# Kernel tuning notes

Measured on AMD Instinct MI355X. Metric: run time of the kernel, lower is better.

The kernel has to match this reference:

```python
import jax, jax.numpy as jnp
import numpy as np

# Module hyperparameters (from init_kwargs)
K = 3          # kernel size
STRIDE = 1
PAD = 1
DIL = 1
DG = 1         # deformable groups
GROUPS = 1     # conv groups


def setup_inputs() -> dict:
    key = jax.random.key(0)
    k1, k2, k3, k4 = jax.random.split(key, 4)
    inputs = jax.random.normal(k1, (8, 64, 96, 96), dtype=jnp.float32)
    offset = jax.random.normal(k2, (8, DG * 2 * K * K, 96, 96), dtype=jnp.float32)
    mask = jax.random.uniform(k3, (8, DG * K * K, 96, 96), dtype=jnp.float32)
    # xavier-ish scale for the conv weight
    weight = jax.random.normal(k4, (64, 64, K, K), dtype=jnp.float32) * 0.05
    return {"inputs": inputs, "offset": offset, "mask": mask, "weight": weight}


def _bilinear_sample(xg, py, px):
    """xg: [N, dg, Cg, H, W]; py, px: [N, dg, P] fractional coords.
    Out-of-bounds samples contribute zero (DCN convention)."""
    N, dg, Cg, H, W = xg.shape
    xf = xg.reshape(N, dg, Cg, H * W)
    y0 = jnp.floor(py)
    x0 = jnp.floor(px)
    wy1 = py - y0
    wx1 = px - x0
    wy0 = 1.0 - wy1
    wx0 = 1.0 - wx1
    y0i = y0.astype(jnp.int32)
    x0i = x0.astype(jnp.int32)
    y1i = y0i + 1
    x1i = x0i + 1

    def gather(yi, xi, w):
        valid = (yi >= 0) & (yi < H) & (xi >= 0) & (xi < W)
        idx = jnp.clip(yi, 0, H - 1) * W + jnp.clip(xi, 0, W - 1)  # [N,dg,P]
        idx_b = jnp.broadcast_to(idx[:, :, None, :], (N, dg, Cg, idx.shape[-1]))
        v = jnp.take_along_axis(xf, idx_b, axis=-1)  # [N,dg,Cg,P]
        return v * (w * valid)[:, :, None, :]

    return (gather(y0i, x0i, wy0 * wx0) + gather(y0i, x1i, wy0 * wx1)
            + gather(y1i, x0i, wy1 * wx0) + gather(y1i, x1i, wy1 * wx1))


def reference(inputs, offset, mask, weight):
    N, C, H, W = inputs.shape
    Cout = weight.shape[0]
    KK = K * K
    Hout = (H + 2 * PAD - DIL * (K - 1) - 1) // STRIDE + 1
    Wout = (W + 2 * PAD - DIL * (K - 1) - 1) // STRIDE + 1

    # offset channels: per deformable group, per kernel tap, (dy, dx) interleaved
    off = offset.reshape(N, DG, KK, 2, Hout, Wout)
    m = mask.reshape(N, DG, KK, Hout, Wout)

    ky, kx = jnp.meshgrid(jnp.arange(K), jnp.arange(K), indexing="ij")
    ky = ky.reshape(KK).astype(jnp.float32)
    kx = kx.reshape(KK).astype(jnp.float32)
    gy = (jnp.arange(Hout) * STRIDE - PAD).astype(jnp.float32)
    gx = (jnp.arange(Wout) * STRIDE - PAD).astype(jnp.float32)
    base_y = ky[:, None, None] * DIL + gy[None, :, None]  # [KK,Hout,1]
    base_x = kx[:, None, None] * DIL + gx[None, None, :]  # [KK,1,Wout]

    py = off[:, :, :, 0] + base_y  # [N,DG,KK,Hout,Wout]
    px = off[:, :, :, 1] + base_x

    P = KK * Hout * Wout
    xg = inputs.reshape(N, DG, C // DG, H, W)
    sampled = _bilinear_sample(xg, py.reshape(N, DG, P), px.reshape(N, DG, P))
    sampled = sampled.reshape(N, DG, C // DG, KK, Hout, Wout) * m[:, :, None]
    cols = sampled.reshape(N, C, KK, Hout, Wout)

    # groups == 1: single GEMM over (C, KK)
    out = jnp.einsum("nckhw,ock->nohw", cols, weight.reshape(Cout, C, KK))
    return out
```

## Files before the change

### kernel.cpp

```cpp
#include <hip/hip_runtime.h>

#define HWX 9216
#define CIN 64
#define COUT 64
#define SR 14
#define SC 24
#define SLOT 144

typedef __attribute__((ext_vector_type(8))) short short8;
typedef __attribute__((ext_vector_type(8))) _Float16 half8;
typedef __attribute__((ext_vector_type(2))) _Float16 half2v;
typedef __attribute__((ext_vector_type(4))) float f32x4;
typedef __attribute__((ext_vector_type(4))) unsigned int u32x4;

__device__ inline unsigned short f2h(float f) {
    union { _Float16 h; unsigned short u; } v;
    v.h = (_Float16)f;
    return v.u;
}
__device__ inline unsigned pack2h(float lo, float hi) {
    return (unsigned)f2h(lo) | ((unsigned)f2h(hi) << 16);
}

__global__ __launch_bounds__(256) void nchw_to_nhwc_f16(const float* __restrict__ x,
                                                        unsigned* __restrict__ xt) {
    __shared__ float tile[64][65];
    int n  = blockIdx.x / 144;
    int p0 = (blockIdx.x % 144) * 64;
    const float* xp = x + (size_t)n * CIN * HWX + p0;
    #pragma unroll
    for (int it = 0; it < 16; ++it) {
        int px = threadIdx.x & 63;
        int c  = (threadIdx.x >> 6) + it * 4;
        tile[c][px] = xp[c * HWX + px];
    }
    __syncthreads();
    unsigned* xo = xt + ((size_t)n * HWX + p0) * 32;
    #pragma unroll
    for (int it = 0; it < 8; ++it) {
        int c2 = threadIdx.x & 31;
        int px = (threadIdx.x >> 5) + it * 8;
        xo[px * 32 + c2] = pack2h(tile[2 * c2][px], tile[2 * c2 + 1][px]);
    }
}

__global__ void dcn_prep_weight(const float* __restrict__ w, unsigned short* __restrict__ wA) {
    int idx = blockIdx.x * blockDim.x + threadIdx.x;
    int j    = idx & 7;
    int lane = (idx >> 3) & 63;
    int m0   = (idx >> 9) & 3;
    int step = idx >> 11;
    int co = m0 * 16 + (lane & 15);
    int kg = step * 32 + ((lane >> 4) << 3) + j;
    int kk = kg >> 6;
    int c  = kg & 63;
    wA[idx] = f2h(w[(co * 64 + c) * 9 + kk]);
}

__global__ __launch_bounds__(384, 4) void dcn_fwd(const unsigned short* __restrict__ xt,
                                                  const float* __restrict__ offset,
                                                  const float* __restrict__ mask,
                                                  const unsigned short* __restrict__ wA,
                                                  float* __restrict__ out) {
    __shared__ __align__(16) char ldsx[SR * SC * SLOT];

    int bid = blockIdx.x;
    int swz = (bid & 7) * 96 + (bid >> 3);
    int n   = swz / 96;
    int t0  = swz % 96;
    int r0  = (t0 / 6) * 6;
    int c0  = (t0 % 6) * 16;

    int sy0 = r0 - 4;
    int sx0 = c0 - 4;

    const unsigned short* xn = xt + (size_t)n * HWX * 64;

    int wave = threadIdx.x >> 6;
    int lane = threadIdx.x & 63;
    int l15  = lane & 15;
    int lg   = lane >> 4;

    int ho = r0 + wave;
    int wo = c0 + l15;

    float dyv[9], dxv[9], mv[9];
    #pragma unroll
    for (int kk = 0; kk < 9; ++kk) {
        dyv[kk] = offset[((n * 18 + 2 * kk + 0) * 96 + ho) * 96 + wo];
        dxv[kk] = offset[((n * 18 + 2 * kk + 1) * 96 + ho) * 96 + wo];
        mv[kk]  = mask[((n * 9 + kk) * 96 + ho) * 96 + wo];
    }

    #pragma unroll
    for (int it = 0; it < 7; ++it) {
        int i  = threadIdx.x + it * 384;
        int s  = i >> 3, ch = i & 7;
        int ly = s / SC, lx = s - ly * SC;
        int gy = min(max(sy0 + ly, 0), 95);
        int gx = min(max(sx0 + lx, 0), 95);
        *(u32x4*)(ldsx + s * SLOT + ch * 16) =
            *((const u32x4*)(xn + (gy * 96 + gx) * 64) + ch);
    }
    __syncthreads();

    f32x4 acc[4] = {f32x4{0,0,0,0}, f32x4{0,0,0,0}, f32x4{0,0,0,0}, f32x4{0,0,0,0}};

    #pragma unroll
    for (int kk = 0; kk < 9; ++kk) {
        int ky = kk / 3, kx = kk % 3;
        float dy = dyv[kk];
        float dx = dxv[kk];
        float m  = mv[kk];

        float py = dy + (float)(ky + ho - 1);
        float px = dx + (float)(kx + wo - 1);
        float y0f = floorf(py), x0f = floorf(px);
        float wy1 = py - y0f,  wx1 = px - x0f;
        float wy0 = 1.f - wy1, wx0 = 1.f - wx1;
        int y0 = (int)y0f, x0 = (int)x0f;
        int y1 = y0 + 1,   x1 = x0 + 1;
        bool vy0 = (y0 >= 0) && (y0 < 96);
        bool vy1 = (y1 >= 0) && (y1 < 96);
        bool vx0 = (x0 >= 0) && (x0 < 96);
        bool vx1 = (x1 >= 0) && (x1 < 96);
        int y0c = min(max(y0, 0), 95), y1c = min(max(y1, 0), 95);
        int x0c = min(max(x0, 0), 95), x1c = min(max(x1, 0), 95);
        float w00 = wy0 * wx0 * m * ((vy0 && vx0) ? 1.f : 0.f);
        float w01 = wy0 * wx1 * m * ((vy0 && vx1) ? 1.f : 0.f);
        float w10 = wy1 * wx0 * m * ((vy1 && vx0) ? 1.f : 0.f);
        float w11 = wy1 * wx1 * m * ((vy1 && vx1) ? 1.f : 0.f);

        _Float16 h00 = (_Float16)w00, h01 = (_Float16)w01;
        _Float16 h10 = (_Float16)w10, h11 = (_Float16)w11;
        half2v W00 = {h00, h00}, W01 = {h01, h01}, W10 = {h10, h10}, W11 = {h11, h11};

        bool local = (y0c >= sy0) & (y1c <= sy0 + SR - 1) &
                     (x0c >= sx0) & (x1c <= sx0 + SC - 1);
        int ly0 = min(max(y0c - sy0, 0), SR - 1);
        int ly1 = min(max(y1c - sy0, 0), SR - 1);
        int lx0 = min(max(x0c - sx0, 0), SC - 1);
        int lx1 = min(max(x1c - sx0, 0), SC - 1);
        int s00 = (ly0 * SC + lx0) * SLOT;
        int s01 = (ly0 * SC + lx1) * SLOT;
        int s10 = (ly1 * SC + lx0) * SLOT;
        int s11 = (ly1 * SC + lx1) * SLOT;

        #pragma unroll
        for (int half = 0; half < 2; ++half) {
            int step = kk * 2 + half;
            int cb   = half * 32 + lg * 8;
            int cb2  = cb * 2;

            const half8* wp = (const half8*)(wA + (step * 256 + lane) * 8);
            half8 af0 = wp[0];
            half8 af1 = wp[64];
            half8 af2 = wp[128];
            half8 af3 = wp[192];

            union { u32x4 u; half2v h[4]; } a00, a01, a10, a11, r;
            a00.u = *(const u32x4*)(ldsx + s00 + cb2);
            a01.u = *(const u32x4*)(ldsx + s01 + cb2);
            a10.u = *(const u32x4*)(ldsx + s10 + cb2);
            a11.u = *(const u32x4*)(ldsx + s11 + cb2);

            if (!local) {
                a00.u = *(const u32x4*)(xn + (y0c * 96 + x0c) * 64 + cb);
                a01.u = *(const u32x4*)(xn + (y0c * 96 + x1c) * 64 + cb);
                a10.u = *(const u32x4*)(xn + (y1c * 96 + x0c) * 64 + cb);
                a11.u = *(const u32x4*)(xn + (y1c * 96 + x1c) * 64 + cb);
            }

            #pragma unroll
            for (int p = 0; p < 4; ++p) {
                r.h[p] = a00.h[p] * W00 + a01.h[p] * W01
                       + a10.h[p] * W10 + a11.h[p] * W11;
            }
            half8 bfrag = *(half8*)&r;

            acc[0] = __builtin_amdgcn_mfma_f32_16x16x32_f16(af0, bfrag, acc[0], 0, 0, 0);
            acc[1] = __builtin_amdgcn_mfma_f32_16x16x32_f16(af1, bfrag, acc[1], 0, 0, 0);
            acc[2] = __builtin_amdgcn_mfma_f32_16x16x32_f16(af2, bfrag, acc[2], 0, 0, 0);
            acc[3] = __builtin_amdgcn_mfma_f32_16x16x32_f16(af3, bfrag, acc[3], 0, 0, 0);
        }
    }

    size_t obase = (size_t)n * COUT * HWX + (size_t)ho * 96 + wo;
    #pragma unroll
    for (int m0 = 0; m0 < 4; ++m0) {
        #pragma unroll
        for (int r = 0; r < 4; ++r) {
            int co = m0 * 16 + lg * 4 + r;
            out[obase + (size_t)co * HWX] = acc[m0][r];
        }
    }
}

extern "C" void kernel_launch(void* const* d_in, const int* in_sizes, int n_in,
                              void* d_out, int out_size, void* d_ws, size_t ws_size,
                              hipStream_t stream) {
    const float* x      = (const float*)d_in[0];
    const float* offset = (const float*)d_in[1];
    const float* mask   = (const float*)d_in[2];
    const float* w      = (const float*)d_in[3];
    float* out = (float*)d_out;
    unsigned* xt       = (unsigned*)d_ws;
    unsigned short* wA = (unsigned short*)((char*)d_ws + (size_t)8 * HWX * 64 * 2);

    hipLaunchKernelGGL(nchw_to_nhwc_f16, dim3(1152), dim3(256), 0, stream, x, xt);
    hipLaunchKernelGGL(dcn_prep_weight, dim3(144), dim3(256), 0, stream, w, wA);
    hipLaunchKernelGGL(dcn_fwd, dim3(768), dim3(384), 0, stream,
                       (const unsigned short*)xt, offset, mask, wA, out);
}
```

Baseline: 34.81 us.

## Software-pipeline bilinear gather one step ahead of MFMA accumulation

Restructures the main tap loop as a software pipeline: the LDS/global corner loads for step u are issued while step u-1's interpolation and MFMAs run, using double-buffered sample and weight registers. Offset and mask values are now loaded one tap ahead instead of all 27 up front, which lowers register pressure. The aim is to hide LDS and global load latency behind MFMA work. In exchange, the live buffers add registers and the compiler may already have scheduled the fully unrolled loop similarly.

```diff
diff --git a/kernel.cpp b/kernel.cpp
--- a/kernel.cpp
+++ b/kernel.cpp
@@ -84,14 +84,6 @@
     int ho = r0 + wave;
     int wo = c0 + l15;
 
-    float dyv[9], dxv[9], mv[9];
-    #pragma unroll
-    for (int kk = 0; kk < 9; ++kk) {
-        dyv[kk] = offset[((n * 18 + 2 * kk + 0) * 96 + ho) * 96 + wo];
-        dxv[kk] = offset[((n * 18 + 2 * kk + 1) * 96 + ho) * 96 + wo];
-        mv[kk]  = mask[((n * 9 + kk) * 96 + ho) * 96 + wo];
-    }
-
     #pragma unroll
     for (int it = 0; it < 7; ++it) {
         int i  = threadIdx.x + it * 384;
@@ -104,84 +96,101 @@
     }
     __syncthreads();
 
+    typedef union { u32x4 u; half2v h[4]; } U;
+
     f32x4 acc[4] = {f32x4{0,0,0,0}, f32x4{0,0,0,0}, f32x4{0,0,0,0}, f32x4{0,0,0,0}};
 
-    #pragma unroll
-    for (int kk = 0; kk < 9; ++kk) {
-        int ky = kk / 3, kx = kk % 3;
-        float dy = dyv[kk];
-        float dx = dxv[kk];
-        float m  = mv[kk];
-
-        float py = dy + (float)(ky + ho - 1);
-        float px = dx + (float)(kx + wo - 1);
-        float y0f = floorf(py), x0f = floorf(px);
-        float wy1 = py - y0f,  wx1 = px - x0f;
-        float wy0 = 1.f - wy1, wx0 = 1.f - wx1;
-        int y0 = (int)y0f, x0 = (int)x0f;
-        int y1 = y0 + 1,   x1 = x0 + 1;
-        bool vy0 = (y0 >= 0) && (y0 < 96);
-        bool vy1 = (y1 >= 0) && (y1 < 96);
-        bool vx0 = (x0 >= 0) && (x0 < 96);
-        bool vx1 = (x1 >= 0) && (x1 < 96);
-        int y0c = min(max(y0, 0), 95), y1c = min(max(y1, 0), 95);
-        int x0c = min(max(x0, 0), 95), x1c = min(max(x1, 0), 95);
-        float w00 = wy0 * wx0 * m * ((vy0 && vx0) ? 1.f : 0.f);
-        float w01 = wy0 * wx1 * m * ((vy0 && vx1) ? 1.f : 0.f);
-        float w10 = wy1 * wx0 * m * ((vy1 && vx0) ? 1.f : 0.f);
-        float w11 = wy1 * wx1 * m * ((vy1 && vx1) ? 1.f : 0.f);
-
-        _Float16 h00 = (_Float16)w00, h01 = (_Float16)w01;
-        _Float16 h10 = (_Float16)w10, h11 = (_Float16)w11;
-        half2v W00 = {h00, h00}, W01 = {h01, h01}, W10 = {h10, h10}, W11 = {h11, h11};
-
-        bool local = (y0c >= sy0) & (y1c <= sy0 + SR - 1) &
-                     (x0c >= sx0) & (x1c <= sx0 + SC - 1);
-        int ly0 = min(max(y0c - sy0, 0), SR - 1);
-        int ly1 = min(max(y1c - sy0, 0), SR - 1);
-        int lx0 = min(max(x0c - sx0, 0), SC - 1);
-        int lx1 = min(max(x1c - sx0, 0), SC - 1);
-        int s00 = (ly0 * SC + lx0) * SLOT;
-        int s01 = (ly0 * SC + lx1) * SLOT;
-        int s10 = (ly1 * SC + lx0) * SLOT;
-        int s11 = (ly1 * SC + lx1) * SLOT;
-
-        #pragma unroll
-        for (int half = 0; half < 2; ++half) {
-            int step = kk * 2 + half;
-            int cb   = half * 32 + lg * 8;
-            int cb2  = cb * 2;
-
-            const half8* wp = (const half8*)(wA + (step * 256 + lane) * 8);
-            half8 af0 = wp[0];
-            half8 af1 = wp[64];
-            half8 af2 = wp[128];
-            half8 af3 = wp[192];
-
-            union { u32x4 u; half2v h[4]; } a00, a01, a10, a11, r;
-            a00.u = *(const u32x4*)(ldsx + s00 + cb2);
-            a01.u = *(const u32x4*)(ldsx + s01 + cb2);
-            a10.u = *(const u32x4*)(ldsx + s10 + cb2);
-            a11.u = *(const u32x4*)(ldsx + s11 + cb2);
-
-            if (!local) {
-                a00.u = *(const u32x4*)(xn + (y0c * 96 + x0c) * 64 + cb);
-                a01.u = *(const u32x4*)(xn + (y0c * 96 + x1c) * 64 + cb);
-                a10.u = *(const u32x4*)(xn + (y1c * 96 + x0c) * 64 + cb);
-                a11.u = *(const u32x4*)(xn + (y1c * 96 + x1c) * 64 + cb);
+    U buf[2][4];
+    half2v Wt[2][4];
+    int sS0 = 0, sS1 = 0, sS2 = 0, sS3 = 0;
+    int gS0 = 0, gS1 = 0, gS2 = 0, gS3 = 0;
+    bool locS = true;
+    float dyn_, dxn_, mn_;
+
+    dyn_ = offset[((n * 18 + 0) * 96 + ho) * 96 + wo];
+    dxn_ = offset[((n * 18 + 1) * 96 + ho) * 96 + wo];
+    mn_  = mask[((n * 9 + 0) * 96 + ho) * 96 + wo];
+
+    #pragma unroll
+    for (int u = 0; u <= 18; ++u) {
+        if (u < 18) {
+            const int tp = u >> 1;
+            const int hp = u & 1;
+            if (hp == 0) {
+                float dy = dyn_, dx = dxn_, mm = mn_;
+                if (tp < 8) {
+                    dyn_ = offset[((n * 18 + 2 * (tp + 1) + 0) * 96 + ho) * 96 + wo];
+                    dxn_ = offset[((n * 18 + 2 * (tp + 1) + 1) * 96 + ho) * 96 + wo];
+                    mn_  = mask[((n * 9 + (tp + 1)) * 96 + ho) * 96 + wo];
+                }
+                float py = dy + (float)(tp / 3 + ho - 1);
+                float px = dx + (float)(tp % 3 + wo - 1);
+                float y0f = floorf(py), x0f = floorf(px);
+                float wy1 = py - y0f, wx1 = px - x0f;
+                float wy0 = 1.f - wy1, wx0 = 1.f - wx1;
+                int y0 = (int)y0f, x0 = (int)x0f;
+                int y1 = y0 + 1, x1 = x0 + 1;
+                bool vy0 = (y0 >= 0) && (y0 < 96);
+                bool vy1 = (y1 >= 0) && (y1 < 96);
+                bool vx0 = (x0 >= 0) && (x0 < 96);
+                bool vx1 = (x1 >= 0) && (x1 < 96);
+                int y0c = min(max(y0, 0), 95), y1c = min(max(y1, 0), 95);
+                int x0c = min(max(x0, 0), 95), x1c = min(max(x1, 0), 95);
+                float w00 = wy0 * wx0 * mm * ((vy0 && vx0) ? 1.f : 0.f);
+                float w01 = wy0 * wx1 * mm * ((vy0 && vx1) ? 1.f : 0.f);
+                float w10 = wy1 * wx0 * mm * ((vy1 && vx0) ? 1.f : 0.f);
+                float w11 = wy1 * wx1 * mm * ((vy1 && vx1) ? 1.f : 0.f);
+                _Float16 h00 = (_Float16)w00, h01 = (_Float16)w01;
+                _Float16 h10 = (_Float16)w10, h11 = (_Float16)w11;
+                Wt[tp & 1][0] = (half2v){h00, h00};
+                Wt[tp & 1][1] = (half2v){h01, h01};
+                Wt[tp & 1][2] = (half2v){h10, h10};
+                Wt[tp & 1][3] = (half2v){h11, h11};
+                locS = (y0c >= sy0) && (y1c <= sy0 + SR - 1) &&
+                       (x0c >= sx0) && (x1c <= sx0 + SC - 1);
+                int ly0 = min(max(y0c - sy0, 0), SR - 1);
+                int ly1 = min(max(y1c - sy0, 0), SR - 1);
+                int lx0 = min(max(x0c - sx0, 0), SC - 1);
+                int lx1 = min(max(x1c - sx0, 0), SC - 1);
+                sS0 = (ly0 * SC + lx0) * SLOT; sS1 = (ly0 * SC + lx1) * SLOT;
+                sS2 = (ly1 * SC + lx0) * SLOT; sS3 = (ly1 * SC + lx1) * SLOT;
+                gS0 = (y0c * 96 + x0c) * 64; gS1 = (y0c * 96 + x1c) * 64;
+                gS2 = (y1c * 96 + x0c) * 64; gS3 = (y1c * 96 + x1c) * 64;
             }
-
-            #pragma unroll
-            for (int p = 0; p < 4; ++p) {
-                r.h[p] = a00.h[p] * W00 + a01.h[p] * W01
-                       + a10.h[p] * W10 + a11.h[p] * W11;
+            {
+                const int oh = hp ? (64 + lg * 16) : (lg * 16);
+                buf[hp][0].u = *(const u32x4*)(ldsx + sS0 + oh);
+                buf[hp][1].u = *(const u32x4*)(ldsx + sS1 + oh);
+                buf[hp][2].u = *(const u32x4*)(ldsx + sS2 + oh);
+                buf[hp][3].u = *(const u32x4*)(ldsx + sS3 + oh);
+                if (__builtin_expect(!locS, 0)) {
+                    const int ch = hp ? (32 + lg * 8) : (lg * 8);
+                    buf[hp][0].u = *(const u32x4*)(xn + gS0 + ch);
+                    buf[hp][1].u = *(const u32x4*)(xn + gS1 + ch);
+                    buf[hp][2].u = *(const u32x4*)(xn + gS2 + ch);
+                    buf[hp][3].u = *(const u32x4*)(xn + gS3 + ch);
+                }
             }
-            half8 bfrag = *(half8*)&r;
-
-            acc[0] = __builtin_amdgcn_mfma_f32_16x16x32_f16(af0, bfrag, acc[0], 0, 0, 0);
-            acc[1] = __builtin_amdgcn_mfma_f32_16x16x32_f16(af1, bfrag, acc[1], 0, 0, 0);
-            acc[2] = __builtin_amdgcn_mfma_f32_16x16x32_f16(af2, bfrag, acc[2], 0, 0, 0);
-            acc[3] = __builtin_amdgcn_mfma_f32_16x16x32_f16(af3, bfrag, acc[3], 0, 0, 0);
+        }
+        if (u > 0) {
+            const int v  = u - 1;
+            const int tc = v >> 1;
+            const int hc = v & 1;
+            U r_;
+            r_.h[0] = buf[hc][0].h[0] * Wt[tc & 1][0] + buf[hc][1].h[0] * Wt[tc & 1][1]
+                    + buf[hc][2].h[0] * Wt[tc & 1][2] + buf[hc][3].h[0] * Wt[tc & 1][3];
+            r_.h[1] = buf[hc][0].h[1] * Wt[tc & 1][0] + buf[hc][1].h[1] * Wt[tc & 1][1]
+                    + buf[hc][2].h[1] * Wt[tc & 1][2] + buf[hc][3].h[1] * Wt[tc & 1][3];
+            r_.h[2] = buf[hc][0].h[2] * Wt[tc & 1][0] + buf[hc][1].h[2] * Wt[tc & 1][1]
+                    + buf[hc][2].h[2] * Wt[tc & 1][2] + buf[hc][3].h[2] * Wt[tc & 1][3];
+            r_.h[3] = buf[hc][0].h[3] * Wt[tc & 1][0] + buf[hc][1].h[3] * Wt[tc & 1][1]
+                    + buf[hc][2].h[3] * Wt[tc & 1][2] + buf[hc][3].h[3] * Wt[tc & 1][3];
+            half8 bf_ = *(half8*)&r_;
+            const half8* wp_ = (const half8*)(wA + ((v) * 256 + lane) * 8);
+            acc[0] = __builtin_amdgcn_mfma_f32_16x16x32_f16(wp_[0],   bf_, acc[0], 0, 0, 0);
+            acc[1] = __builtin_amdgcn_mfma_f32_16x16x32_f16(wp_[64],  bf_, acc[1], 0, 0, 0);
+            acc[2] = __builtin_amdgcn_mfma_f32_16x16x32_f16(wp_[128], bf_, acc[2], 0, 0, 0);
+            acc[3] = __builtin_amdgcn_mfma_f32_16x16x32_f16(wp_[192], bf_, acc[3], 0, 0, 0);
         }
     }
 
```

Measured after the change: 38.07 us. 9.4% more time.
